# Kernel tuning notes

Hardware: AMD Instinct MI355X
Metric: run time of the kernel (lower is better)

## Reference

```python
import jax, jax.numpy as jnp
import numpy as np
import math

B, S, DM, H = 4, 2048, 1024, 16
HD = DM // H

def setup_inputs() -> dict:
    key = jax.random.key(0)
    ks = jax.random.split(key, 12)
    def lin(k, din, dout):
        bound = 1.0 / math.sqrt(din)
        kw, kb = jax.random.split(k)
        W = jax.random.uniform(kw, (din, dout), jnp.float32, -bound, bound)
        b = jax.random.uniform(kb, (dout,), jnp.float32, -bound, bound)
        return W, b
    Wq, bq = lin(ks[0], DM, DM)
    Wk, bk = lin(ks[1], DM, DM)
    Wv, bv = lin(ks[2], DM, DM)
    Wo, bo = lin(ks[3], DM, DM)
    return {
        "Q": jax.random.normal(ks[4], (B, S, DM), jnp.float32),
        "K": jax.random.normal(ks[5], (B, S, DM), jnp.float32),
        "V": jax.random.normal(ks[6], (B, S, DM), jnp.float32),
        "mask": jnp.ones((B, S), jnp.int32),
        "Wq": Wq, "bq": bq, "Wk": Wk, "bk": bk,
        "Wv": Wv, "bv": bv, "Wo": Wo, "bo": bo,
    }

def reference(Q, K, V, mask, Wq, bq, Wk, bk, Wv, bv, Wo, bo):
    N, qlen, dm = Q.shape
    klen = K.shape[1]
    q = (Q @ Wq + bq).reshape(N, qlen, H, HD)
    k = (K @ Wk + bk).reshape(N, klen, H, HD)
    v = (V @ Wv + bv).reshape(N, klen, H, HD)
    # scores: [B, q, H, k]
    dot = jnp.einsum('bqhd,bkhd->bqhk', q, k) / math.sqrt(HD)
    # mask is 2-D (N, klen): broadcast as (N, 1, 1, klen); positions where mask==0 are masked
    m = (mask == 0)[:, None, None, :]
    dot = jnp.where(m, -jnp.inf, dot)
    weights = jax.nn.softmax(dot.astype(jnp.float32), axis=-1).astype(dot.dtype)
    out = jnp.einsum('bqhk,bkhd->bqhd', weights, v).reshape(N, qlen, dm)
    return out @ Wo + bo
```

## Files before the change

### kernel.cpp

```cpp
#include <hip/hip_runtime.h>
#include <math.h>

#define B_  4
#define S_  2048
#define DM_ 1024
#define H_  16
#define HD_ 64

typedef float f32x4 __attribute__((ext_vector_type(4)));
typedef short bf16x8 __attribute__((ext_vector_type(8)));

#define MFMA16(a, b, c) __builtin_amdgcn_mfma_f32_16x16x32_bf16((a), (b), (c), 0, 0, 0)

static __device__ __forceinline__ unsigned short f2bf(float f) {
    union { float f; unsigned int i; } c; c.f = f;
    unsigned int u = c.i;
    return (unsigned short)((u + 0x7fffu + ((u >> 16) & 1u)) >> 16);
}
static __device__ __forceinline__ unsigned int f2u(float f) {
    union { float f; unsigned int u; } c; c.f = f; return c.u;
}

static __device__ __forceinline__ void async16(const void* g, void* l) {
    __builtin_amdgcn_global_load_lds(
        (__attribute__((address_space(1))) void*)(void*)g,
        (__attribute__((address_space(3))) void*)l, 16, 0, 0);
}

__global__ __launch_bounds__(256) void cast3_bf16(
    const float* __restrict__ q, const float* __restrict__ k,
    const float* __restrict__ v,
    unsigned short* __restrict__ qo, unsigned short* __restrict__ ko,
    unsigned short* __restrict__ vo) {
    const int z = blockIdx.z;
    const float* in = z == 0 ? q : (z == 1 ? k : v);
    unsigned short* out = z == 0 ? qo : (z == 1 ? ko : vo);
    int idx = (blockIdx.x * 256 + threadIdx.x) * 8;
    float4 a = *(const float4*)(in + idx);
    float4 b = *(const float4*)(in + idx + 4);
    *(ushort4*)(out + idx)     = make_ushort4(f2bf(a.x), f2bf(a.y), f2bf(a.z), f2bf(a.w));
    *(ushort4*)(out + idx + 4) = make_ushort4(f2bf(b.x), f2bf(b.y), f2bf(b.z), f2bf(b.w));
}

__global__ __launch_bounds__(256) void wcast4_t(
    const float* __restrict__ w0, const float* __restrict__ w1,
    const float* __restrict__ w2, const float* __restrict__ w3,
    unsigned short* __restrict__ o0, unsigned short* __restrict__ o1,
    unsigned short* __restrict__ o2, unsigned short* __restrict__ o3) {
    __shared__ float tile[64][65];
    const int z = blockIdx.z;
    const float* W = z == 0 ? w0 : (z == 1 ? w1 : (z == 2 ? w2 : w3));
    unsigned short* Wt = z == 0 ? o0 : (z == 1 ? o1 : (z == 2 ? o2 : o3));
    const int t = threadIdx.x;
    const int k0 = blockIdx.y * 64, n0 = blockIdx.x * 64;
    const int r = t >> 4, c4 = (t & 15) * 4;
    #pragma unroll
    for (int s = 0; s < 4; ++s) {
        float4 f = *(const float4*)(W + (size_t)(k0 + s * 16 + r) * DM_ + n0 + c4);
        tile[s * 16 + r][c4 + 0] = f.x; tile[s * 16 + r][c4 + 1] = f.y;
        tile[s * 16 + r][c4 + 2] = f.z; tile[s * 16 + r][c4 + 3] = f.w;
    }
    __syncthreads();
    #pragma unroll
    for (int s = 0; s < 4; ++s) {
        int n = s * 16 + r;
        ushort4 o = make_ushort4(f2bf(tile[c4 + 0][n]), f2bf(tile[c4 + 1][n]),
                                 f2bf(tile[c4 + 2][n]), f2bf(tile[c4 + 3][n]));
        *(ushort4*)(Wt + (size_t)(n0 + n) * DM_ + k0 + c4) = o;
    }
}

static __device__ __forceinline__ void gemm_body(
    const unsigned short* __restrict__ A,
    const unsigned short* __restrict__ Wt,
    const float* __restrict__ bias,
    void* __restrict__ outp, int mode,
    unsigned short* As, unsigned short* Bs)
{
    const int t = threadIdx.x;
    const int w = t >> 6, l = t & 63;
    const int quad = l >> 4, l16 = l & 15;
    const int wr = w >> 1, wc = w & 1;
    const int m0 = blockIdx.y * 128, n0 = blockIdx.x * 128;

    const int srow8 = l >> 3;
    const int sch   = (l & 7) ^ srow8;
    const unsigned short* ag = A  + (size_t)(m0 + w * 32 + srow8) * DM_ + sch * 8;
    const unsigned short* bg = Wt + (size_t)(n0 + w * 32 + srow8) * DM_ + sch * 8;

    const f32x4 fz = {0.f, 0.f, 0.f, 0.f};
    f32x4 acc[4][4];
    #pragma unroll
    for (int i = 0; i < 4; ++i)
        #pragma unroll
        for (int j = 0; j < 4; ++j) acc[i][j] = fz;

    const int rsw = l16 & 7;
    for (int k0 = 0; k0 < DM_; k0 += 64) {
        __syncthreads();
        #pragma unroll
        for (int s = 0; s < 4; ++s) {
            async16(ag + k0 + (size_t)(s * 8) * DM_, &As[(w * 32 + s * 8) * 64]);
            async16(bg + k0 + (size_t)(s * 8) * DM_, &Bs[(w * 32 + s * 8) * 64]);
        }
        __syncthreads();
        #pragma unroll
        for (int c = 0; c < 2; ++c) {
            const int csw = ((c * 4 + quad) ^ rsw) * 8;
            bf16x8 af[4], bfr[4];
            #pragma unroll
            for (int i = 0; i < 4; ++i)
                af[i] = *(const bf16x8*)&As[(wr * 64 + i * 16 + l16) * 64 + csw];
            #pragma unroll
            for (int j = 0; j < 4; ++j)
                bfr[j] = *(const bf16x8*)&Bs[(wc * 64 + j * 16 + l16) * 64 + csw];
            #pragma unroll
            for (int i = 0; i < 4; ++i)
                #pragma unroll
                for (int j = 0; j < 4; ++j)
                    acc[i][j] = MFMA16(af[i], bfr[j], acc[i][j]);
        }
    }

    float bv[4];
    #pragma unroll
    for (int j = 0; j < 4; ++j) bv[j] = bias[n0 + wc * 64 + j * 16 + l16];

    if (mode == 2) {
        float* out = (float*)outp;
        #pragma unroll
        for (int i = 0; i < 4; ++i)
            #pragma unroll
            for (int j = 0; j < 4; ++j) {
                int col = n0 + wc * 64 + j * 16 + l16;
                #pragma unroll
                for (int r = 0; r < 4; ++r) {
                    int row = m0 + wr * 64 + i * 16 + quad * 4 + r;
                    out[(size_t)row * DM_ + col] = acc[i][j][r] + bv[j];
                }
            }
    } else if (mode == 0) {
        unsigned short* out = (unsigned short*)outp;
        #pragma unroll
        for (int i = 0; i < 4; ++i)
            #pragma unroll
            for (int j = 0; j < 4; ++j) {
                int col = n0 + wc * 64 + j * 16 + l16;
                int h = col >> 6, d = col & 63;
                #pragma unroll
                for (int r = 0; r < 4; ++r) {
                    int row = m0 + wr * 64 + i * 16 + quad * 4 + r;
                    int bb = row >> 11, ss = row & (S_ - 1);
                    out[(((size_t)bb * H_ + h) * S_ + ss) * HD_ + d] =
                        f2bf(acc[i][j][r] + bv[j]);
                }
            }
    } else {
        unsigned short* out = (unsigned short*)outp;
        #pragma unroll
        for (int i = 0; i < 4; ++i)
            #pragma unroll
            for (int j = 0; j < 4; ++j) {
                int col = n0 + wc * 64 + j * 16 + l16;
                int h = col >> 6, d = col & 63;
                int row0 = m0 + wr * 64 + i * 16 + quad * 4;
                int bb = row0 >> 11, ss = row0 & (S_ - 1);
                ushort4 o = make_ushort4(f2bf(acc[i][j][0] + bv[j]),
                                         f2bf(acc[i][j][1] + bv[j]),
                                         f2bf(acc[i][j][2] + bv[j]),
                                         f2bf(acc[i][j][3] + bv[j]));
                *(ushort4*)(out + (((size_t)bb * H_ + h) * HD_ + d) * S_ + ss) = o;
            }
    }
}

__global__ __launch_bounds__(256) void gemm_qkv3(
    const unsigned short* __restrict__ Qc, const unsigned short* __restrict__ Kc,
    const unsigned short* __restrict__ Vc,
    const unsigned short* __restrict__ Wqt, const unsigned short* __restrict__ Wkt,
    const unsigned short* __restrict__ Wvt,
    const float* __restrict__ bq, const float* __restrict__ bk,
    const float* __restrict__ bvp,
    unsigned short* __restrict__ qh, unsigned short* __restrict__ kh,
    unsigned short* __restrict__ vth)
{
    __shared__ unsigned short As[128 * 64];
    __shared__ unsigned short Bs[128 * 64];
    const int z = blockIdx.z;
    const unsigned short* A  = z == 0 ? Qc  : (z == 1 ? Kc  : Vc);
    const unsigned short* Wt = z == 0 ? Wqt : (z == 1 ? Wkt : Wvt);
    const float* bias        = z == 0 ? bq  : (z == 1 ? bk  : bvp);
    void* out                = z == 0 ? (void*)qh : (z == 1 ? (void*)kh : (void*)vth);
    gemm_body(A, Wt, bias, out, z == 2 ? 1 : 0, As, Bs);
}

__global__ __launch_bounds__(256) void gemm_omfma(
    const unsigned short* __restrict__ A, const unsigned short* __restrict__ Wt,
    const float* __restrict__ bias, float* __restrict__ out)
{
    __shared__ unsigned short As[128 * 64];
    __shared__ unsigned short Bs[128 * 64];
    gemm_body(A, Wt, bias, out, 2, As, Bs);
}

__global__ __launch_bounds__(256) void attn_mfma(
    const unsigned short* __restrict__ q,
    const unsigned short* __restrict__ k,
    const unsigned short* __restrict__ vt,
    const int* __restrict__ mask,
    unsigned short* __restrict__ out)
{
    __shared__ unsigned short Qs[128 * 64];
    __shared__ unsigned short Ks[64 * 64];
    __shared__ unsigned short Vs[64 * 64];
    __shared__ unsigned short Ps[4][2][16 * 64];
    __shared__ float msf[64];
    const int t = threadIdx.x;
    const int w = t >> 6, l = t & 63;
    const int quad = l >> 4, l16 = l & 15;
    const int b = blockIdx.z, h = blockIdx.y;
    const int q0 = blockIdx.x * 128;
    const size_t hb = ((size_t)b * H_ + h) * S_;
    const float C_ = 0.18033688011112042f;
    const float NINF = -__builtin_inff();

    const int srow8 = l >> 3;
    const int sch   = (l & 7) ^ srow8;

    const unsigned short* qg = q + (hb + q0) * HD_;
    #pragma unroll
    for (int s = 0; s < 4; ++s) {
        int r0 = w * 32 + s * 8;
        async16(qg + (size_t)(r0 + srow8) * HD_ + sch * 8, &Qs[r0 * 64]);
    }
    __syncthreads();
    bf16x8 qf[2][2];
    #pragma unroll
    for (int g = 0; g < 2; ++g)
        #pragma unroll
        for (int c = 0; c < 2; ++c) {
            int row = w * 32 + g * 16 + l16;
            qf[g][c] = *(const bf16x8*)&Qs[row * 64 + (((c * 4 + quad) ^ (row & 7)) * 8)];
        }

    const f32x4 fz = {0.f, 0.f, 0.f, 0.f};
    f32x4 o[2][4];
    float lr[2] = {0.f, 0.f};
    #pragma unroll
    for (int g = 0; g < 2; ++g)
        #pragma unroll
        for (int jv = 0; jv < 4; ++jv) o[g][jv] = fz;

    const unsigned short* kg0 = k + hb * HD_;
    const unsigned short* vg0 = vt + ((size_t)b * H_ + h) * HD_ * S_;
    const int rsw = l16 & 7;

    for (int kt = 0; kt < S_ / 64; ++kt) {
        __syncthreads();
        #pragma unroll
        for (int s = 0; s < 2; ++s) {
            int r0 = w * 16 + s * 8;
            int rr = r0 + srow8;
            async16(kg0 + (size_t)(kt * 64 + rr) * HD_ + sch * 8, &Ks[r0 * 64]);
            async16(vg0 + (size_t)rr * S_ + kt * 64 + sch * 8, &Vs[r0 * 64]);
        }
        if (t < 64) msf[t] = mask[(size_t)b * S_ + kt * 64 + t] ? 0.f : NINF;
        __syncthreads();

        float madd[4][4];
        #pragma unroll
        for (int kk = 0; kk < 4; ++kk) {
            float4 mv = *(const float4*)&msf[kk * 16 + quad * 4];
            madd[kk][0] = mv.x; madd[kk][1] = mv.y;
            madd[kk][2] = mv.z; madd[kk][3] = mv.w;
        }

        bf16x8 kf[4][2], vfr[4][2];
        #pragma unroll
        for (int kk = 0; kk < 4; ++kk) {
            int row = kk * 16 + l16;
            #pragma unroll
            for (int c = 0; c < 2; ++c)
                kf[kk][c] = *(const bf16x8*)&Ks[row * 64 + (((c * 4 + quad) ^ rsw) * 8)];
        }
        #pragma unroll
        for (int jv = 0; jv < 4; ++jv) {
            int row = jv * 16 + l16;
            #pragma unroll
            for (int c = 0; c < 2; ++c)
                vfr[jv][c] = *(const bf16x8*)&Vs[row * 64 + (((c * 4 + quad) ^ rsw) * 8)];
        }

        #pragma unroll
        for (int g = 0; g < 2; ++g) {
            f32x4 sc[4];
            #pragma unroll
            for (int kk = 0; kk < 4; ++kk) sc[kk] = fz;
            #pragma unroll
            for (int kk = 0; kk < 4; ++kk) {
                sc[kk] = MFMA16(kf[kk][0], qf[g][0], sc[kk]);
                sc[kk] = MFMA16(kf[kk][1], qf[g][1], sc[kk]);
            }
            unsigned short* Pg = &Ps[w][g][0];
            float lacc = 0.f;
            #pragma unroll
            for (int kk = 0; kk < 4; ++kk) {
                int kb = (kk * 2 + (quad >> 1)) ^ rsw;
                #pragma unroll
                for (int rp = 0; rp < 2; ++rp) {
                    float p0 = __builtin_amdgcn_exp2f(
                        fmaf(sc[kk][rp * 2 + 0], C_, madd[kk][rp * 2 + 0]));
                    float p1 = __builtin_amdgcn_exp2f(
                        fmaf(sc[kk][rp * 2 + 1], C_, madd[kk][rp * 2 + 1]));
                    unsigned int pk = __builtin_amdgcn_perm(f2u(p1), f2u(p0), 0x07060302u);
                    lacc += p0 + p1;
                    *(unsigned int*)&Pg[l16 * 64 + kb * 8 + (quad & 1) * 4 + rp * 2] = pk;
                }
            }
            lr[g] += lacc;
            bf16x8 pa0 = *(const bf16x8*)&Pg[l16 * 64 + ((quad ^ rsw) * 8)];
            bf16x8 pa1 = *(const bf16x8*)&Pg[l16 * 64 + (((4 + quad) ^ rsw) * 8)];
            #pragma unroll
            for (int jv = 0; jv < 4; ++jv) {
                o[g][jv] = MFMA16(pa0, vfr[jv][0], o[g][jv]);
                o[g][jv] = MFMA16(pa1, vfr[jv][1], o[g][jv]);
            }
        }
    }
    #pragma unroll
    for (int g = 0; g < 2; ++g) {
        float ls = lr[g];
        ls += __shfl_xor(ls, 16);
        ls += __shfl_xor(ls, 32);
        float inv = 1.0f / ls;
        float invr[4];
        #pragma unroll
        for (int r = 0; r < 4; ++r)
            invr[r] = __shfl(inv, (l & 48) | (quad * 4 + r));
        #pragma unroll
        for (int jv = 0; jv < 4; ++jv) {
            int col = h * HD_ + jv * 16 + l16;
            #pragma unroll
            for (int r = 0; r < 4; ++r) {
                int row = q0 + w * 32 + g * 16 + quad * 4 + r;
                out[((size_t)b * S_ + row) * DM_ + col] = f2bf(o[g][jv][r] * invr[r]);
            }
        }
    }
}

extern "C" void kernel_launch(void* const* d_in, const int* in_sizes, int n_in,
                              void* d_out, int out_size, void* d_ws, size_t ws_size,
                              hipStream_t stream) {
    const float* Q    = (const float*)d_in[0];
    const float* K    = (const float*)d_in[1];
    const float* V    = (const float*)d_in[2];
    const int*   mask = (const int*)d_in[3];
    const float* Wq   = (const float*)d_in[4];
    const float* bq   = (const float*)d_in[5];
    const float* Wk   = (const float*)d_in[6];
    const float* bk   = (const float*)d_in[7];
    const float* Wv   = (const float*)d_in[8];
    const float* bv   = (const float*)d_in[9];
    const float* Wo   = (const float*)d_in[10];
    const float* bo   = (const float*)d_in[11];

    char* ws = (char*)d_ws;
    const size_t MB = 1024 * 1024;
    unsigned short* Qc  = (unsigned short*)(ws);
    unsigned short* Kc  = (unsigned short*)(ws + 16 * MB);
    unsigned short* Vc  = (unsigned short*)(ws + 32 * MB);
    unsigned short* Wqt = (unsigned short*)(ws + 48 * MB);
    unsigned short* Wkt = (unsigned short*)(ws + 50 * MB);
    unsigned short* Wvt = (unsigned short*)(ws + 52 * MB);
    unsigned short* Wot = (unsigned short*)(ws + 54 * MB);
    unsigned short* qh  = (unsigned short*)(ws + 56 * MB);
    unsigned short* kh  = (unsigned short*)(ws + 72 * MB);
    unsigned short* vth = (unsigned short*)(ws + 88 * MB);
    unsigned short* ao  = (unsigned short*)(ws + 104 * MB);

    cast3_bf16<<<dim3(4096, 1, 3), 256, 0, stream>>>(Q, K, V, Qc, Kc, Vc);
    wcast4_t<<<dim3(16, 16, 4), 256, 0, stream>>>(Wq, Wk, Wv, Wo, Wqt, Wkt, Wvt, Wot);
    gemm_qkv3<<<dim3(DM_ / 128, (B_ * S_) / 128, 3), 256, 0, stream>>>(
        Qc, Kc, Vc, Wqt, Wkt, Wvt, bq, bk, bv, qh, kh, vth);
    attn_mfma<<<dim3(S_ / 128, H_, B_), 256, 0, stream>>>(qh, kh, vth, mask, ao);
    gemm_omfma<<<dim3(DM_ / 128, (B_ * S_) / 128), 256, 0, stream>>>(ao, Wot, bo, (float*)d_out);
}
```

Measured before the change: 359.4 us.

## Double-buffer K/V in attention, fold softmax scale into Q, precompute mask flags

The attention kernel now double-buffers K/V tiles in LDS, prefetching the next tile while computing the current one, and removes one barrier per iteration. The softmax scale (1/sqrt(d)·log2 e) is folded into the Q projection epilogue. A small prep kernel turns the mask into additive floats plus per-64-key all-valid flags so unmasked tiles skip the mask add. Q fragments load directly from global memory, the grid is flattened with a block swizzle, and the kernel gets a 4-blocks-per-CU launch bound. The risks are higher register pressure under the occupancy bound and slight rounding changes from scaling q before the bf16 cast.

```diff
diff --git a/kernel.cpp b/kernel.cpp
--- a/kernel.cpp
+++ b/kernel.cpp
@@ -42,6 +42,17 @@
     *(ushort4*)(out + idx + 4) = make_ushort4(f2bf(b.x), f2bf(b.y), f2bf(b.z), f2bf(b.w));
 }
 
+__global__ __launch_bounds__(256) void maskprep(
+    const int* __restrict__ mask, float* __restrict__ maddf,
+    unsigned int* __restrict__ flags) {
+    int i = blockIdx.x * 256 + threadIdx.x;
+    int m = mask[i];
+    maddf[i] = m ? 0.f : -__builtin_inff();
+    unsigned long long bal = __ballot(m != 0);
+    if ((threadIdx.x & 63) == 0)
+        flags[i >> 6] = (bal == 0xFFFFFFFFFFFFFFFFull) ? 1u : 0u;
+}
+
 __global__ __launch_bounds__(256) void wcast4_t(
     const float* __restrict__ w0, const float* __restrict__ w1,
     const float* __restrict__ w2, const float* __restrict__ w3,
@@ -74,7 +85,7 @@
     const unsigned short* __restrict__ A,
     const unsigned short* __restrict__ Wt,
     const float* __restrict__ bias,
-    void* __restrict__ outp, int mode,
+    void* __restrict__ outp, int mode, float oscale,
     unsigned short* As, unsigned short* Bs)
 {
     const int t = threadIdx.x;
@@ -152,7 +163,7 @@
                     int row = m0 + wr * 64 + i * 16 + quad * 4 + r;
                     int bb = row >> 11, ss = row & (S_ - 1);
                     out[(((size_t)bb * H_ + h) * S_ + ss) * HD_ + d] =
-                        f2bf(acc[i][j][r] + bv[j]);
+                        f2bf((acc[i][j][r] + bv[j]) * oscale);
                 }
             }
     } else {
@@ -191,7 +202,8 @@
     const unsigned short* Wt = z == 0 ? Wqt : (z == 1 ? Wkt : Wvt);
     const float* bias        = z == 0 ? bq  : (z == 1 ? bk  : bvp);
     void* out                = z == 0 ? (void*)qh : (z == 1 ? (void*)kh : (void*)vth);
-    gemm_body(A, Wt, bias, out, z == 2 ? 1 : 0, As, Bs);
+    const float qsc = 0.18033688011112042f;
+    gemm_body(A, Wt, bias, out, z == 2 ? 1 : 0, z == 0 ? qsc : 1.0f, As, Bs);
 }
 
 __global__ __launch_bounds__(256) void gemm_omfma(
@@ -200,48 +212,65 @@
 {
     __shared__ unsigned short As[128 * 64];
     __shared__ unsigned short Bs[128 * 64];
-    gemm_body(A, Wt, bias, out, 2, As, Bs);
-}
-
-__global__ __launch_bounds__(256) void attn_mfma(
+    gemm_body(A, Wt, bias, out, 2, 1.0f, As, Bs);
+}
+
+template<bool MASKED>
+static __device__ __forceinline__ void softmax_store(
+    const f32x4* sc, const float (*madd)[4], unsigned short* Pg,
+    int l16, int quad, int rsw, float& lout)
+{
+    float lacc = 0.f;
+    #pragma unroll
+    for (int kk = 0; kk < 4; ++kk) {
+        int kb = (kk * 2 + (quad >> 1)) ^ rsw;
+        #pragma unroll
+        for (int rp = 0; rp < 2; ++rp) {
+            float a0 = sc[kk][rp * 2 + 0], a1 = sc[kk][rp * 2 + 1];
+            if (MASKED) { a0 += madd[kk][rp * 2 + 0]; a1 += madd[kk][rp * 2 + 1]; }
+            float p0 = __builtin_amdgcn_exp2f(a0);
+            float p1 = __builtin_amdgcn_exp2f(a1);
+            unsigned int pk = __builtin_amdgcn_perm(f2u(p1), f2u(p0), 0x07060302u);
+            lacc += p0 + p1;
+            *(unsigned int*)&Pg[l16 * 64 + kb * 8 + (quad & 1) * 4 + rp * 2] = pk;
+        }
+    }
+    lout += lacc;
+}
+
+__global__ __launch_bounds__(256, 4) void attn_mfma(
     const unsigned short* __restrict__ q,
     const unsigned short* __restrict__ k,
     const unsigned short* __restrict__ vt,
-    const int* __restrict__ mask,
+    const float* __restrict__ maddf,
+    const unsigned int* __restrict__ flags,
     unsigned short* __restrict__ out)
 {
-    __shared__ unsigned short Qs[128 * 64];
-    __shared__ unsigned short Ks[64 * 64];
-    __shared__ unsigned short Vs[64 * 64];
-    __shared__ unsigned short Ps[4][2][16 * 64];
-    __shared__ float msf[64];
+    __shared__ unsigned short Ks[2][64 * 64];
+    __shared__ unsigned short Vs[2][64 * 64];
+    __shared__ unsigned short Ps[4][16 * 64];
     const int t = threadIdx.x;
     const int w = t >> 6, l = t & 63;
     const int quad = l >> 4, l16 = l & 15;
-    const int b = blockIdx.z, h = blockIdx.y;
-    const int q0 = blockIdx.x * 128;
+
+    const int bid = blockIdx.x;
+    const int swz = (bid & 7) * 128 + (bid >> 3);
+    const int qb = swz & 15, h = (swz >> 4) & 15, b = swz >> 8;
+    const int q0 = qb * 128;
     const size_t hb = ((size_t)b * H_ + h) * S_;
-    const float C_ = 0.18033688011112042f;
-    const float NINF = -__builtin_inff();
 
     const int srow8 = l >> 3;
     const int sch   = (l & 7) ^ srow8;
+    const int rsw   = l16 & 7;
 
     const unsigned short* qg = q + (hb + q0) * HD_;
-    #pragma unroll
-    for (int s = 0; s < 4; ++s) {
-        int r0 = w * 32 + s * 8;
-        async16(qg + (size_t)(r0 + srow8) * HD_ + sch * 8, &Qs[r0 * 64]);
-    }
-    __syncthreads();
     bf16x8 qf[2][2];
     #pragma unroll
     for (int g = 0; g < 2; ++g)
         #pragma unroll
-        for (int c = 0; c < 2; ++c) {
-            int row = w * 32 + g * 16 + l16;
-            qf[g][c] = *(const bf16x8*)&Qs[row * 64 + (((c * 4 + quad) ^ (row & 7)) * 8)];
-        }
+        for (int c = 0; c < 2; ++c)
+            qf[g][c] = *(const bf16x8*)(qg +
+                (size_t)(w * 32 + g * 16 + l16) * HD_ + (c * 4 + quad) * 8);
 
     const f32x4 fz = {0.f, 0.f, 0.f, 0.f};
     f32x4 o[2][4];
@@ -253,42 +282,51 @@
 
     const unsigned short* kg0 = k + hb * HD_;
     const unsigned short* vg0 = vt + ((size_t)b * H_ + h) * HD_ * S_;
-    const int rsw = l16 & 7;
-
-    for (int kt = 0; kt < S_ / 64; ++kt) {
-        __syncthreads();
+    unsigned short* Pg = &Ps[w][0];
+
+    auto stage = [&](int d, int kt) {
         #pragma unroll
         for (int s = 0; s < 2; ++s) {
             int r0 = w * 16 + s * 8;
             int rr = r0 + srow8;
-            async16(kg0 + (size_t)(kt * 64 + rr) * HD_ + sch * 8, &Ks[r0 * 64]);
-            async16(vg0 + (size_t)rr * S_ + kt * 64 + sch * 8, &Vs[r0 * 64]);
-        }
-        if (t < 64) msf[t] = mask[(size_t)b * S_ + kt * 64 + t] ? 0.f : NINF;
+            async16(kg0 + (size_t)(kt * 64 + rr) * HD_ + sch * 8, &Ks[d][r0 * 64]);
+            async16(vg0 + (size_t)rr * S_ + kt * 64 + sch * 8, &Vs[d][r0 * 64]);
+        }
+    };
+
+    stage(0, 0);
+    int cur = 0;
+    for (int kt = 0; kt < S_ / 64; ++kt) {
         __syncthreads();
-
+        if (kt + 1 < S_ / 64) stage(cur ^ 1, kt + 1);
+
+        const int allv = flags[b * (S_ / 64) + kt];
         float madd[4][4];
-        #pragma unroll
-        for (int kk = 0; kk < 4; ++kk) {
-            float4 mv = *(const float4*)&msf[kk * 16 + quad * 4];
-            madd[kk][0] = mv.x; madd[kk][1] = mv.y;
-            madd[kk][2] = mv.z; madd[kk][3] = mv.w;
-        }
-
+        if (!allv) {
+            #pragma unroll
+            for (int kk = 0; kk < 4; ++kk) {
+                float4 mv = *(const float4*)&maddf[(size_t)b * S_ + kt * 64 + kk * 16 + quad * 4];
+                madd[kk][0] = mv.x; madd[kk][1] = mv.y;
+                madd[kk][2] = mv.z; madd[kk][3] = mv.w;
+            }
+        }
+
+        const unsigned short* Kc = &Ks[cur][0];
+        const unsigned short* Vc = &Vs[cur][0];
         bf16x8 kf[4][2], vfr[4][2];
         #pragma unroll
         for (int kk = 0; kk < 4; ++kk) {
             int row = kk * 16 + l16;
             #pragma unroll
             for (int c = 0; c < 2; ++c)
-                kf[kk][c] = *(const bf16x8*)&Ks[row * 64 + (((c * 4 + quad) ^ rsw) * 8)];
+                kf[kk][c] = *(const bf16x8*)&Kc[row * 64 + (((c * 4 + quad) ^ rsw) * 8)];
         }
         #pragma unroll
         for (int jv = 0; jv < 4; ++jv) {
             int row = jv * 16 + l16;
             #pragma unroll
             for (int c = 0; c < 2; ++c)
-                vfr[jv][c] = *(const bf16x8*)&Vs[row * 64 + (((c * 4 + quad) ^ rsw) * 8)];
+                vfr[jv][c] = *(const bf16x8*)&Vc[row * 64 + (((c * 4 + quad) ^ rsw) * 8)];
         }
 
         #pragma unroll
@@ -301,23 +339,9 @@
                 sc[kk] = MFMA16(kf[kk][0], qf[g][0], sc[kk]);
                 sc[kk] = MFMA16(kf[kk][1], qf[g][1], sc[kk]);
             }
-            unsigned short* Pg = &Ps[w][g][0];
-            float lacc = 0.f;
-            #pragma unroll
-            for (int kk = 0; kk < 4; ++kk) {
-                int kb = (kk * 2 + (quad >> 1)) ^ rsw;
-                #pragma unroll
-                for (int rp = 0; rp < 2; ++rp) {
-                    float p0 = __builtin_amdgcn_exp2f(
-                        fmaf(sc[kk][rp * 2 + 0], C_, madd[kk][rp * 2 + 0]));
-                    float p1 = __builtin_amdgcn_exp2f(
-                        fmaf(sc[kk][rp * 2 + 1], C_, madd[kk][rp * 2 + 1]));
-                    unsigned int pk = __builtin_amdgcn_perm(f2u(p1), f2u(p0), 0x07060302u);
-                    lacc += p0 + p1;
-                    *(unsigned int*)&Pg[l16 * 64 + kb * 8 + (quad & 1) * 4 + rp * 2] = pk;
-                }
-            }
-            lr[g] += lacc;
+            if (allv) softmax_store<false>(sc, madd, Pg, l16, quad, rsw, lr[g]);
+            else      softmax_store<true >(sc, madd, Pg, l16, quad, rsw, lr[g]);
+
             bf16x8 pa0 = *(const bf16x8*)&Pg[l16 * 64 + ((quad ^ rsw) * 8)];
             bf16x8 pa1 = *(const bf16x8*)&Pg[l16 * 64 + (((4 + quad) ^ rsw) * 8)];
             #pragma unroll
@@ -326,7 +350,9 @@
                 o[g][jv] = MFMA16(pa1, vfr[jv][1], o[g][jv]);
             }
         }
-    }
+        cur ^= 1;
+    }
+
     #pragma unroll
     for (int g = 0; g < 2; ++g) {
         float ls = lr[g];
@@ -378,11 +404,15 @@
     unsigned short* kh  = (unsigned short*)(ws + 72 * MB);
     unsigned short* vth = (unsigned short*)(ws + 88 * MB);
     unsigned short* ao  = (unsigned short*)(ws + 104 * MB);
+    float*          maddf = (float*)(ws + 120 * MB);
+    unsigned int*   flagsb = (unsigned int*)(ws + 120 * MB + 64 * 1024);
 
     cast3_bf16<<<dim3(4096, 1, 3), 256, 0, stream>>>(Q, K, V, Qc, Kc, Vc);
+    maskprep<<<dim3((B_ * S_) / 256), 256, 0, stream>>>(mask, maddf, flagsb);
     wcast4_t<<<dim3(16, 16, 4), 256, 0, stream>>>(Wq, Wk, Wv, Wo, Wqt, Wkt, Wvt, Wot);
     gemm_qkv3<<<dim3(DM_ / 128, (B_ * S_) / 128, 3), 256, 0, stream>>>(
         Qc, Kc, Vc, Wqt, Wkt, Wvt, bq, bk, bv, qh, kh, vth);
-    attn_mfma<<<dim3(S_ / 128, H_, B_), 256, 0, stream>>>(qh, kh, vth, mask, ao);
+    attn_mfma<<<dim3((S_ / 128) * H_ * B_), 256, 0, stream>>>(
+        qh, kh, vth, maddf, flagsb, ao);
     gemm_omfma<<<dim3(DM_ / 128, (B_ * S_) / 128), 256, 0, stream>>>(ao, Wot, bo, (float*)d_out);
 }
```

New measurement: 642.3 us. 1.79x slower.
